# Optimization experiments

Hardware: AMD Instinct MI355X
Metric: run time of the kernel (lower is better)

Reference implementation:

```python
import jax, jax.numpy as jnp
import numpy as np

NH = 16   # num heads
CS = 16   # inner chunk size

def _gelu(x):
    return jax.nn.gelu(x, approximate=True)

def _diff_gelu(x):
    t = jnp.tanh(0.79788456 * x * (1.0 + 0.044715 * x * x))
    return 0.5 * x * ((1.0 - t * t) * (0.79788456 + 0.1070322243 * x * x)) + 0.5 * (1.0 + t)

def _ln_fused_l2_bwd(x, tgt, gamma, beta, eps=1e-6):
    # x, tgt: [B*nh, CS, f]; gamma/beta: [1, nh, 1, f]
    Bnh, N, HF = x.shape
    mu = x.mean(-1, keepdims=True)
    var = x.var(-1, keepdims=True)
    std = jnp.sqrt(var + eps)
    x_hat = (x - mu) / std
    y = gamma * x_hat.reshape(-1, NH, N, HF) + beta
    go = y - tgt.reshape(-1, NH, N, HF)
    gxh = (go * gamma).reshape(Bnh, N, HF)
    return (HF * gxh - gxh.sum(-1, keepdims=True) - x_hat * (gxh * x_hat).sum(-1, keepdims=True)) / (HF * std)

def setup_inputs() -> dict:
    key = jax.random.key(0)
    ks = jax.random.split(key, 8)
    B, nh, f, hf4, n_chunks = 4, NH, 64, 256, 128
    Bnh = B * nh
    XQ = jax.random.normal(ks[0], (n_chunks, Bnh, CS, f), jnp.float32)
    XK = jax.random.normal(ks[1], (n_chunks, Bnh, CS, f), jnp.float32)
    XV = jax.random.normal(ks[2], (n_chunks, Bnh, CS, f), jnp.float32)
    # inner-loop lr coeffs (ilr * token_idx ~ lr/head_dim): small positive
    coeff = jax.random.uniform(ks[3], (n_chunks, Bnh, CS, 1), jnp.float32) * 0.01
    coeff_last = jax.random.uniform(ks[4], (n_chunks, Bnh, 1, 1), jnp.float32) * 0.01
    W1 = jax.random.normal(ks[5], (Bnh, f, hf4), jnp.float32) * 0.02
    b1 = jnp.zeros((Bnh, 1, hf4), jnp.float32)
    W2 = jax.random.normal(ks[6], (Bnh, hf4, f), jnp.float32) * 0.02
    b2 = jnp.zeros((Bnh, 1, f), jnp.float32)
    ln_weight = jnp.ones((1, nh, 1, f), jnp.float32)
    ln_bias = jnp.zeros((1, nh, 1, f), jnp.float32)
    return dict(XQ=XQ, XK=XK, XV=XV, coeff=coeff, coeff_last=coeff_last,
                W1=W1, b1=b1, W2=W2, b2=b2, ln_weight=ln_weight, ln_bias=ln_bias)

def reference(XQ, XK, XV, coeff, coeff_last, W1, b1, W2, b2, ln_weight, ln_bias):
    n_chunks, Bnh, _, f = XQ.shape
    attn_b = jnp.tril(jnp.ones((CS, CS), XQ.dtype))

    def step(carry, inp):
        W1c, b1c, W2c, b2c = carry
        xv, xk, xq, c, cl = inp
        Z1 = xk @ W1c + b1c                      # [Bnh, CS, 4f]
        X2 = _gelu(Z1)
        Z2 = X2 @ W2c + b2c                      # [Bnh, CS, f]
        dZ2 = _ln_fused_l2_bwd(Z2, xv - xk, ln_weight, ln_bias)
        dZ1 = (dZ2 @ W2c.transpose(0, 2, 1)) * _diff_gelu(Z1)
        b1_bar = b1c - c * (attn_b @ dZ1)
        A1 = jnp.tril(xq @ xk.transpose(0, 2, 1))
        Z1_bar = xq @ W1c - c * (A1 @ dZ1) + b1_bar
        X2_bar = _gelu(Z1_bar)
        b2_bar = b2c - c * (attn_b @ dZ2)
        A2 = jnp.tril(X2_bar @ X2.transpose(0, 2, 1))
        Z2_bar = X2_bar @ W2c - c * (A2 @ dZ2) + b2_bar
        W1n = W1c - cl * (xk.transpose(0, 2, 1) @ dZ1)
        W2n = W2c - cl * (X2.transpose(0, 2, 1) @ dZ2)
        return (W1n, b1_bar[:, -1:], W2n, b2_bar[:, -1:]), Z2_bar

    _, Z2_all = jax.lax.scan(step, (W1, b1, W2, b2), (XV, XK, XQ, coeff, coeff_last))
    # [n_chunks, Bnh, CS, f] -> [Bnh, N, f]
    return Z2_all.transpose(1, 0, 2, 3).reshape(Bnh, n_chunks * CS, f)
```

## Files before the change

kernel.cpp:

```cpp
#include <hip/hip_runtime.h>

typedef __attribute__((ext_vector_type(8))) short bf16x8;
typedef __attribute__((ext_vector_type(4))) float f32x4;
typedef __attribute__((ext_vector_type(2))) unsigned int u32x2;

#define MFMA16(a,b,c) __builtin_amdgcn_mfma_f32_16x16x32_bf16(a,b,c,0,0,0)
#define A_GELU 0.7978845608028654f

#define OFF_W1B   0u
#define OFF_W2F   36864u
#define OFF_W2T   70656u
#define OFF_XK    107520u
#define OFF_XQ    109824u
#define OFF_XKT   112128u
#define OFF_X2    115200u
#define OFF_X2B   123648u
#define OFF_DZ2B  132096u
#define OFF_DZ1CT 134400u
#define OFF_DZ2CT 146688u
#define OFF_M1    149760u
#define OFF_M2    150528u
#define OFF_Z2F   151296u
#define OFF_Z2G   155520u
#define OFF_TGT   159744u
#define OFF_B2    162048u
#define OFF_COEF  162560u
#define OFF_CL    162624u
#define SMEM_BYTES 162640u

__device__ __forceinline__ float fast_tanh(float u){
    float e = __expf(2.0f*u);
    return 1.0f - 2.0f/(e + 1.0f);
}
__device__ __forceinline__ float gelu_f(float x){
    float t = fast_tanh(A_GELU*(x + 0.044715f*x*x*x));
    return 0.5f*x*(1.0f+t);
}
__device__ __forceinline__ float dgelu_f(float x){
    float x2 = x*x;
    float t = fast_tanh(A_GELU*x*(1.0f + 0.044715f*x2));
    return 0.5f*x*((1.0f-t*t)*(A_GELU + 0.1070322243f*x2)) + 0.5f*(1.0f+t);
}
__device__ __forceinline__ short f2bf(float f){
    unsigned u = __builtin_bit_cast(unsigned, f);
    u += 0x7FFFu + ((u >> 16) & 1u);
    return (short)(u >> 16);
}
__device__ __forceinline__ float bf2f(unsigned short s){
    unsigned u = ((unsigned)s) << 16;
    return __builtin_bit_cast(float, u);
}
__device__ __forceinline__ unsigned pkbf(float a, float b){
    unsigned r;
    asm("v_cvt_pk_bf16_f32 %0, %1, %2" : "=v"(r) : "v"(a), "v"(b));
    return r;
}
__device__ __forceinline__ bf16x8 ldfrag(const unsigned short* p){
    return *(const bf16x8*)p;
}
__device__ __forceinline__ bf16x8 ldmask16(const unsigned short* row, int hi){
    bf16x8 r = {0,0,0,0,0,0,0,0};
    if (hi < 2) r = *(const bf16x8*)(row + hi*8);
    return r;
}

__global__ __launch_bounds__(512, 1)
void ttt_m2(const float* __restrict__ XQ, const float* __restrict__ XK,
            const float* __restrict__ XV, const float* __restrict__ coeff,
            const float* __restrict__ coeff_last,
            const float* __restrict__ W1g, const float* __restrict__ b1g,
            const float* __restrict__ W2g, const float* __restrict__ b2g,
            const float* __restrict__ gammag, const float* __restrict__ betag,
            float* __restrict__ out)
{
    const int h  = blockIdx.x;
    const int t  = threadIdx.x;
    const int l  = t & 63;
    const int w  = t >> 6;
    const int lo = l & 15;
    const int hi = l >> 4;

    extern __shared__ char smem[];
    unsigned short* sW1bu  = (unsigned short*)(smem + OFF_W1B);
    unsigned short* sW2fu  = (unsigned short*)(smem + OFF_W2F);
    unsigned short* sW2T   = (unsigned short*)(smem + OFF_W2T);
    unsigned short* sxku   = (unsigned short*)(smem + OFF_XK);
    unsigned short* sxqu   = (unsigned short*)(smem + OFF_XQ);
    unsigned short* sxkT   = (unsigned short*)(smem + OFF_XKT);
    unsigned short* sX2u   = (unsigned short*)(smem + OFF_X2);
    unsigned short* sX2bu  = (unsigned short*)(smem + OFF_X2B);
    unsigned short* sdZ2bu = (unsigned short*)(smem + OFF_DZ2B);
    unsigned short* sdZ1ct = (unsigned short*)(smem + OFF_DZ1CT);
    unsigned short* sdZ2ct = (unsigned short*)(smem + OFF_DZ2CT);
    unsigned short* sM1u   = (unsigned short*)(smem + OFF_M1);
    unsigned short* sM2u   = (unsigned short*)(smem + OFF_M2);
    float* sZ2f  = (float*)(smem + OFF_Z2F);
    float* sZ2g  = (float*)(smem + OFF_Z2G);
    unsigned short* stgtu = (unsigned short*)(smem + OFF_TGT);
    float* b2f   = (float*)(smem + OFF_B2);
    float* scoef = (float*)(smem + OFF_COEF);
    float* sCL   = (float*)(smem + OFF_CL);

    const int base1 = h*16384;
    const int base2 = h*16384;

    float mW1[4][2][4];
    float mW2[2][4][4];
    #pragma unroll
    for (int mt = 0; mt < 4; ++mt)
      #pragma unroll
      for (int tix = 0; tix < 2; ++tix)
        #pragma unroll
        for (int reg = 0; reg < 4; ++reg) {
            const int m = mt*16 + hi*4 + reg, n = (2*w + tix)*16 + lo;
            mW1[mt][tix][reg] = W1g[base1 + m*256 + n];
        }
    #pragma unroll
    for (int mi = 0; mi < 2; ++mi)
      #pragma unroll
      for (int nt = 0; nt < 4; ++nt)
        #pragma unroll
        for (int reg = 0; reg < 4; ++reg) {
            const int m = (2*w + mi)*16 + hi*4 + reg, n = nt*16 + lo;
            mW2[mi][nt][reg] = W2g[base2 + m*64 + n];
        }
    float b1reg[2];
    b1reg[0] = b1g[h*256 + (2*w)*16 + lo];
    b1reg[1] = b1g[h*256 + (2*w+1)*16 + lo];

    for (int i = 0; i < 32; ++i) {
        const int idx = i*512 + t;
        const int m = idx >> 8, n = idx & 255;
        sW1bu[n*72 + m] = f2bf(W1g[base1 + idx]);
    }
    for (int i = 0; i < 32; ++i) {
        const int idx = i*512 + t;
        const int hf = idx >> 6, f = idx & 63;
        const short v = f2bf(W2g[base2 + idx]);
        sW2fu[f*264 + hf] = v;
        sW2T[hf*72 + f]   = v;
    }
    if (t < 64) b2f[t] = b2g[h*64 + t];

    const float gj = gammag[(h & 15)*64 + l];
    const float bj = betag [(h & 15)*64 + l];

    {
        const int r0 = w*2;
        const float xk0 = XK[h*1024 + r0*64 + l],     xq0 = XQ[h*1024 + r0*64 + l];
        const float xk1 = XK[h*1024 + (r0+1)*64 + l], xq1 = XQ[h*1024 + (r0+1)*64 + l];
        const float xv0 = XV[h*1024 + r0*64 + l],     xv1 = XV[h*1024 + (r0+1)*64 + l];
        const unsigned pkk = pkbf(xk0, xk1), pkq = pkbf(xq0, xq1);
        const unsigned pkt = pkbf(xv0 - xk0, xv1 - xk1);
        sxku[r0*72 + l]     = (unsigned short)pkk;
        sxku[(r0+1)*72 + l] = (unsigned short)(pkk >> 16);
        sxqu[r0*72 + l]     = (unsigned short)pkq;
        sxqu[(r0+1)*72 + l] = (unsigned short)(pkq >> 16);
        *(unsigned*)&sxkT[l*24 + r0] = pkk;
        stgtu[r0*72 + l]     = (unsigned short)pkt;
        stgtu[(r0+1)*72 + l] = (unsigned short)(pkt >> 16);
        if (t < 16)  scoef[t] = coeff[h*16 + t];
        if (t == 16) sCL[0]   = coeff_last[h];
    }
    __syncthreads();

    for (int ci = 0; ci < 128; ++ci) {
        const float clv = sCL[0];
        const float c15 = scoef[15];
        float crs[4];
        #pragma unroll
        for (int reg = 0; reg < 4; ++reg) crs[reg] = scoef[hi*4 + reg];

        float pxk[4], pxq[4], pxv[4];
        float pcf = 0.f, pcl = 0.f;
        if (w >= 4 && ci < 127) {
            const int cb1 = (ci + 1)*65536 + h*1024;
            const int r0 = (w - 4)*4;
            #pragma unroll
            for (int i = 0; i < 4; ++i) {
                pxk[i] = XK[cb1 + (r0 + i)*64 + l];
                pxq[i] = XQ[cb1 + (r0 + i)*64 + l];
                pxv[i] = XV[cb1 + (r0 + i)*64 + l];
            }
            const int u = t - 256;
            if (u < 16)  pcf = coeff[(ci + 1)*1024 + h*16 + u];
            if (u == 16) pcl = coeff_last[(ci + 1)*64 + h];
        }

        float z1s[8];
        bf16x8 afk0 = ldfrag(sxku + lo*72 + hi*8);
        bf16x8 afk1 = ldfrag(sxku + lo*72 + 32 + hi*8);
        #pragma unroll
        for (int tix = 0; tix < 2; ++tix) {
            const int n = (2*w + tix)*16 + lo;
            f32x4 acc = {b1reg[tix], b1reg[tix], b1reg[tix], b1reg[tix]};
            acc = MFMA16(afk0, ldfrag(sW1bu + n*72 + hi*8), acc);
            acc = MFMA16(afk1, ldfrag(sW1bu + n*72 + 32 + hi*8), acc);
            float g[4];
            #pragma unroll
            for (int reg = 0; reg < 4; ++reg) {
                z1s[tix*4 + reg] = acc[reg];
                g[reg] = gelu_f(acc[reg]);
            }
            const unsigned p01 = pkbf(g[0], g[1]), p23 = pkbf(g[2], g[3]);
            sX2u[(hi*4+0)*264 + n] = (unsigned short)p01;
            sX2u[(hi*4+1)*264 + n] = (unsigned short)(p01 >> 16);
            sX2u[(hi*4+2)*264 + n] = (unsigned short)p23;
            sX2u[(hi*4+3)*264 + n] = (unsigned short)(p23 >> 16);
        }
        if (w == 0) {
            bf16x8 aq0 = ldfrag(sxqu + lo*72 + hi*8);
            bf16x8 aq1 = ldfrag(sxqu + lo*72 + 32 + hi*8);
            f32x4 a1 = {0.f, 0.f, 0.f, 0.f};
            a1 = MFMA16(aq0, afk0, a1);
            a1 = MFMA16(aq1, afk1, a1);
            #pragma unroll
            for (int reg = 0; reg < 4; ++reg) {
                const int r = hi*4 + reg;
                const float v = (lo <= r) ? (-crs[reg]*(a1[reg] + 1.0f)) : 0.0f;
                sM1u[r*24 + lo] = f2bf(v);
            }
        }
        #pragma unroll
        for (int mi = 0; mi < 2; ++mi)
          #pragma unroll
          for (int nt = 0; nt < 4; ++nt) {
                const int n = nt*16 + lo, m0 = (2*w + mi)*16 + hi*4;
                const unsigned p01 = pkbf(mW2[mi][nt][0], mW2[mi][nt][1]);
                const unsigned p23 = pkbf(mW2[mi][nt][2], mW2[mi][nt][3]);
                *(u32x2*)&sW2fu[n*264 + m0] = (u32x2){p01, p23};
                sW2T[(m0+0)*72 + n] = (unsigned short)p01;
                sW2T[(m0+1)*72 + n] = (unsigned short)(p01 >> 16);
                sW2T[(m0+2)*72 + n] = (unsigned short)p23;
                sW2T[(m0+3)*72 + n] = (unsigned short)(p23 >> 16);
          }
        __syncthreads();

        const int tile = w & 3, kh = w >> 2;
        const int nf = tile*16 + lo;
        {
            f32x4 acc;
            if (kh == 0) {
                const float b2v = b2f[(ci & 1)*64 + nf];
                acc = (f32x4){b2v, b2v, b2v, b2v};
            } else acc = (f32x4){0.f, 0.f, 0.f, 0.f};
            #pragma unroll
            for (int s = 0; s < 4; ++s) {
                const int k = (kh*4 + s)*32 + hi*8;
                acc = MFMA16(ldfrag(sX2u + lo*264 + k),
                             ldfrag(sW2fu + nf*264 + k), acc);
            }
            float* dst = (kh == 0) ? sZ2g : sZ2f;
            #pragma unroll
            for (int reg = 0; reg < 4; ++reg)
                dst[(hi*4 + reg)*66 + nf] = acc[reg];
        }
        __syncthreads();

        {
            float dzp[2];
            #pragma unroll
            for (int i = 0; i < 2; ++i) {
                const int r = w*2 + i;
                const float z2 = sZ2f[r*66 + l] + sZ2g[r*66 + l];
                float s1 = z2, s2 = z2*z2;
                #pragma unroll
                for (int m = 1; m < 64; m <<= 1) { s1 += __shfl_xor(s1, m); s2 += __shfl_xor(s2, m); }
                const float mu   = s1*(1.0f/64.0f);
                const float var  = s2*(1.0f/64.0f) - mu*mu;
                const float rstd = rsqrtf(var + 1e-6f);
                const float xh   = (z2 - mu)*rstd;
                const float go   = gj*xh + bj - bf2f(stgtu[r*72 + l]);
                const float gg   = go*gj;
                float u1 = gg, u2 = gg*xh;
                #pragma unroll
                for (int m = 1; m < 64; m <<= 1) { u1 += __shfl_xor(u1, m); u2 += __shfl_xor(u2, m); }
                dzp[i] = (64.0f*gg - u1 - xh*u2)*(rstd*(1.0f/64.0f));
            }
            const unsigned pk = pkbf(dzp[0], dzp[1]);
            sdZ2bu[(w*2)*72 + l]   = (unsigned short)pk;
            sdZ2bu[(w*2+1)*72 + l] = (unsigned short)(pk >> 16);
            *(unsigned*)&sdZ2ct[l*24 + w*2] = pk;
        }
        __syncthreads();

        float b1old[2];
        {
            bf16x8 ad0 = ldfrag(sdZ2bu + lo*72 + hi*8);
            bf16x8 ad1 = ldfrag(sdZ2bu + lo*72 + 32 + hi*8);
            #pragma unroll
            for (int tix = 0; tix < 2; ++tix) {
                const int n = (2*w + tix)*16 + lo;
                f32x4 acc = {0.f, 0.f, 0.f, 0.f};
                acc = MFMA16(ad0, ldfrag(sW2T + n*72 + hi*8), acc);
                acc = MFMA16(ad1, ldfrag(sW2T + n*72 + 32 + hi*8), acc);
                float dv[4], cs = 0.f;
                #pragma unroll
                for (int reg = 0; reg < 4; ++reg) {
                    dv[reg] = acc[reg]*dgelu_f(z1s[tix*4 + reg]);
                    cs += dv[reg];
                }
                *(u32x2*)&sdZ1ct[n*24 + hi*4] =
                    (u32x2){pkbf(dv[0], dv[1]), pkbf(dv[2], dv[3])};
                cs += __shfl_xor(cs, 16);
                cs += __shfl_xor(cs, 32);
                b1old[tix] = b1reg[tix];
                b1reg[tix] -= c15*cs;
            }
        }
        __syncthreads();

        {
            bf16x8 aq0 = ldfrag(sxqu + lo*72 + hi*8);
            bf16x8 aq1 = ldfrag(sxqu + lo*72 + 32 + hi*8);
            bf16x8 am1 = ldmask16(sM1u + lo*24, hi);
            #pragma unroll
            for (int tix = 0; tix < 2; ++tix) {
                const int n = (2*w + tix)*16 + lo;
                f32x4 acc = {b1old[tix], b1old[tix], b1old[tix], b1old[tix]};
                acc = MFMA16(aq0, ldfrag(sW1bu + n*72 + hi*8), acc);
                acc = MFMA16(aq1, ldfrag(sW1bu + n*72 + 32 + hi*8), acc);
                acc = MFMA16(am1, ldmask16(sdZ1ct + n*24, hi), acc);
                float g[4];
                #pragma unroll
                for (int reg = 0; reg < 4; ++reg) g[reg] = gelu_f(acc[reg]);
                const unsigned p01 = pkbf(g[0], g[1]), p23 = pkbf(g[2], g[3]);
                sX2bu[(hi*4+0)*264 + n] = (unsigned short)p01;
                sX2bu[(hi*4+1)*264 + n] = (unsigned short)(p01 >> 16);
                sX2bu[(hi*4+2)*264 + n] = (unsigned short)p23;
                sX2bu[(hi*4+3)*264 + n] = (unsigned short)(p23 >> 16);
            }
            bf16x8 bz0 = ldmask16(sdZ1ct + ((2*w)*16 + lo)*24, hi);
            bf16x8 bz1 = ldmask16(sdZ1ct + ((2*w+1)*16 + lo)*24, hi);
            #pragma unroll
            for (int mt = 0; mt < 4; ++mt) {
                bf16x8 axt = ldmask16(sxkT + (mt*16 + lo)*24, hi);
                f32x4 z4 = {0.f,0.f,0.f,0.f};
                f32x4 u0 = MFMA16(axt, bz0, z4);
                f32x4 u1 = MFMA16(axt, bz1, z4);
                #pragma unroll
                for (int reg = 0; reg < 4; ++reg) {
                    mW1[mt][0][reg] -= clv*u0[reg];
                    mW1[mt][1][reg] -= clv*u1[reg];
                }
            }
        }
        __syncthreads();

        {
            bf16x8 bz2[4];
            #pragma unroll
            for (int nt = 0; nt < 4; ++nt)
                bz2[nt] = ldmask16(sdZ2ct + (nt*16 + lo)*24, hi);
            #pragma unroll
            for (int mi = 0; mi < 2; ++mi) {
                const int mt = 2*w + mi;
                bf16x8 ax2 = (bf16x8){0,0,0,0,0,0,0,0};
                if (l < 32) {
                    #pragma unroll
                    for (int j = 0; j < 8; ++j)
                        ax2[j] = (short)sX2u[(hi*8 + j)*264 + (mt*16 + lo)];
                }
                #pragma unroll
                for (int nt = 0; nt < 4; ++nt) {
                    f32x4 z4 = {0.f,0.f,0.f,0.f};
                    f32x4 u = MFMA16(ax2, bz2[nt], z4);
                    #pragma unroll
                    for (int reg = 0; reg < 4; ++reg)
                        mW2[mi][nt][reg] -= clv*u[reg];
                }
            }
            if (w == 0) {
                f32x4 a2 = {0.f,0.f,0.f,0.f};
                #pragma unroll
                for (int ks = 0; ks < 8; ++ks) {
                    const int k = ks*32 + hi*8;
                    a2 = MFMA16(ldfrag(sX2bu + lo*264 + k),
                                ldfrag(sX2u + lo*264 + k), a2);
                }
                #pragma unroll
                for (int reg = 0; reg < 4; ++reg) {
                    const int r = hi*4 + reg;
                    const float v = (lo <= r) ? (-crs[reg]*(a2[reg] + 1.0f)) : 0.0f;
                    sM2u[r*24 + lo] = f2bf(v);
                }
            }
            if (w == 1) {
                float cs = 0.f;
                #pragma unroll
                for (int k = 0; k < 16; ++k) cs += bf2f(sdZ2bu[k*72 + l]);
                b2f[((ci + 1) & 1)*64 + l] = b2f[(ci & 1)*64 + l] - c15*cs;
            }
            #pragma unroll
            for (int mt = 0; mt < 4; ++mt)
              #pragma unroll
              for (int tix = 0; tix < 2; ++tix) {
                    const int n = (2*w + tix)*16 + lo, m0 = mt*16 + hi*4;
                    *(u32x2*)&sW1bu[n*72 + m0] =
                        (u32x2){pkbf(mW1[mt][tix][0], mW1[mt][tix][1]),
                                pkbf(mW1[mt][tix][2], mW1[mt][tix][3])};
              }
        }
        __syncthreads();

        if (w < 4) {
            const int nf2 = w*16 + lo;
            const float b2v = b2f[(ci & 1)*64 + nf2];
            f32x4 acc = {b2v, b2v, b2v, b2v};
            #pragma unroll
            for (int s = 0; s < 8; ++s) {
                const int k0 = s*32 + hi*8;
                acc = MFMA16(ldfrag(sX2bu + lo*264 + k0),
                             ldfrag(sW2fu + nf2*264 + k0), acc);
            }
            acc = MFMA16(ldmask16(sM2u + lo*24, hi),
                         ldmask16(sdZ2ct + nf2*24, hi), acc);
            #pragma unroll
            for (int reg = 0; reg < 4; ++reg)
                out[h*131072 + (ci*16 + hi*4 + reg)*64 + nf2] = acc[reg];
        } else if (ci < 127) {
            const int r0 = (w - 4)*4;
            #pragma unroll
            for (int p = 0; p < 2; ++p) {
                const int r = r0 + 2*p;
                const unsigned pkk = pkbf(pxk[2*p], pxk[2*p+1]);
                const unsigned pkq = pkbf(pxq[2*p], pxq[2*p+1]);
                const unsigned pkt = pkbf(pxv[2*p] - pxk[2*p], pxv[2*p+1] - pxk[2*p+1]);
                sxku[r*72 + l]     = (unsigned short)pkk;
                sxku[(r+1)*72 + l] = (unsigned short)(pkk >> 16);
                sxqu[r*72 + l]     = (unsigned short)pkq;
                sxqu[(r+1)*72 + l] = (unsigned short)(pkq >> 16);
                *(unsigned*)&sxkT[l*24 + r] = pkk;
                stgtu[r*72 + l]     = (unsigned short)pkt;
                stgtu[(r+1)*72 + l] = (unsigned short)(pkt >> 16);
            }
            const int u = t - 256;
            if (u < 16)  scoef[u] = pcf;
            if (u == 16) sCL[0]   = pcl;
        }
        __syncthreads();
    }
}

extern "C" void kernel_launch(void* const* d_in, const int* in_sizes, int n_in,
                              void* d_out, int out_size, void* d_ws, size_t ws_size,
                              hipStream_t stream) {
    const float* XQ  = (const float*)d_in[0];
    const float* XK  = (const float*)d_in[1];
    const float* XV  = (const float*)d_in[2];
    const float* cf  = (const float*)d_in[3];
    const float* cfl = (const float*)d_in[4];
    const float* W1  = (const float*)d_in[5];
    const float* b1  = (const float*)d_in[6];
    const float* W2  = (const float*)d_in[7];
    const float* b2  = (const float*)d_in[8];
    const float* gam = (const float*)d_in[9];
    const float* bet = (const float*)d_in[10];
    float* o = (float*)d_out;

    hipFuncSetAttribute((const void*)ttt_m2,
                        hipFuncAttributeMaxDynamicSharedMemorySize, SMEM_BYTES);
    ttt_m2<<<64, 512, SMEM_BYTES, stream>>>(XQ, XK, XV, cf, cfl, W1, b1, W2, b2, gam, bet, o);
}
```

Measured before the change: 866.9 us.

## Keep a transposed W2 copy in registers and build X2 fragments via shuffles

Adds a second register-resident copy of W2 in transposed fragment layout, updated by its own MFMAs each chunk. The transposed shared-memory copy of W2 can then be written with packed 8-byte stores instead of four scalar 2-byte stores. The X2 operand for the W2 update is now built from the GELU values kept in registers, using cross-lane shuffles rather than strided scalar LDS reads. In exchange it uses 32 more registers per thread and eight more MFMAs per chunk, which could lower occupancy or cause spills.

After: 1.497 ms. +72.7%, slower.

```diff
diff --git a/kernel.cpp b/kernel.cpp
--- a/kernel.cpp
+++ b/kernel.cpp
@@ -3,6 +3,7 @@
 typedef __attribute__((ext_vector_type(8))) short bf16x8;
 typedef __attribute__((ext_vector_type(4))) float f32x4;
 typedef __attribute__((ext_vector_type(2))) unsigned int u32x2;
+typedef __attribute__((ext_vector_type(4))) unsigned int u32x4;
 
 #define MFMA16(a,b,c) __builtin_amdgcn_mfma_f32_16x16x32_bf16(a,b,c,0,0,0)
 #define A_GELU 0.7978845608028654f
@@ -106,6 +107,7 @@
 
     float mW1[4][2][4];
     float mW2[2][4][4];
+    float mW2T[4][2][4];
     #pragma unroll
     for (int mt = 0; mt < 4; ++mt)
       #pragma unroll
@@ -123,6 +125,15 @@
         for (int reg = 0; reg < 4; ++reg) {
             const int m = (2*w + mi)*16 + hi*4 + reg, n = nt*16 + lo;
             mW2[mi][nt][reg] = W2g[base2 + m*64 + n];
+        }
+    #pragma unroll
+    for (int ft = 0; ft < 4; ++ft)
+      #pragma unroll
+      for (int tix = 0; tix < 2; ++tix)
+        #pragma unroll
+        for (int reg = 0; reg < 4; ++reg) {
+            const int f = ft*16 + hi*4 + reg, hf = (2*w + tix)*16 + lo;
+            mW2T[ft][tix][reg] = W2g[base2 + hf*64 + f];
         }
     float b1reg[2];
     b1reg[0] = b1g[h*256 + (2*w)*16 + lo];
@@ -188,6 +199,7 @@
         }
 
         float z1s[8];
+        unsigned px2[2][2];
         bf16x8 afk0 = ldfrag(sxku + lo*72 + hi*8);
         bf16x8 afk1 = ldfrag(sxku + lo*72 + 32 + hi*8);
         #pragma unroll
@@ -203,6 +215,7 @@
                 g[reg] = gelu_f(acc[reg]);
             }
             const unsigned p01 = pkbf(g[0], g[1]), p23 = pkbf(g[2], g[3]);
+            px2[tix][0] = p01; px2[tix][1] = p23;
             sX2u[(hi*4+0)*264 + n] = (unsigned short)p01;
             sX2u[(hi*4+1)*264 + n] = (unsigned short)(p01 >> 16);
             sX2u[(hi*4+2)*264 + n] = (unsigned short)p23;
@@ -226,13 +239,18 @@
           #pragma unroll
           for (int nt = 0; nt < 4; ++nt) {
                 const int n = nt*16 + lo, m0 = (2*w + mi)*16 + hi*4;
-                const unsigned p01 = pkbf(mW2[mi][nt][0], mW2[mi][nt][1]);
-                const unsigned p23 = pkbf(mW2[mi][nt][2], mW2[mi][nt][3]);
-                *(u32x2*)&sW2fu[n*264 + m0] = (u32x2){p01, p23};
-                sW2T[(m0+0)*72 + n] = (unsigned short)p01;
-                sW2T[(m0+1)*72 + n] = (unsigned short)(p01 >> 16);
-                sW2T[(m0+2)*72 + n] = (unsigned short)p23;
-                sW2T[(m0+3)*72 + n] = (unsigned short)(p23 >> 16);
+                *(u32x2*)&sW2fu[n*264 + m0] =
+                    (u32x2){pkbf(mW2[mi][nt][0], mW2[mi][nt][1]),
+                            pkbf(mW2[mi][nt][2], mW2[mi][nt][3])};
+          }
+        #pragma unroll
+        for (int ft = 0; ft < 4; ++ft)
+          #pragma unroll
+          for (int tix = 0; tix < 2; ++tix) {
+                const int hf = (2*w + tix)*16 + lo, f0 = ft*16 + hi*4;
+                *(u32x2*)&sW2T[hf*72 + f0] =
+                    (u32x2){pkbf(mW2T[ft][tix][0], mW2T[ft][tix][1]),
+                            pkbf(mW2T[ft][tix][2], mW2T[ft][tix][3])};
           }
         __syncthreads();
 
@@ -352,24 +370,39 @@
             #pragma unroll
             for (int nt = 0; nt < 4; ++nt)
                 bz2[nt] = ldmask16(sdZ2ct + (nt*16 + lo)*24, hi);
-            #pragma unroll
-            for (int mi = 0; mi < 2; ++mi) {
-                const int mt = 2*w + mi;
-                bf16x8 ax2 = (bf16x8){0,0,0,0,0,0,0,0};
-                if (l < 32) {
-                    #pragma unroll
-                    for (int j = 0; j < 8; ++j)
-                        ax2[j] = (short)sX2u[(hi*8 + j)*264 + (mt*16 + lo)];
-                }
+            bf16x8 xf[2];
+            {
+                const int base = lo + 32*(hi & 1);
+                #pragma unroll
+                for (int tix = 0; tix < 2; ++tix) {
+                    unsigned w0 = (unsigned)__shfl((int)px2[tix][0], base);
+                    unsigned w1 = (unsigned)__shfl((int)px2[tix][1], base);
+                    unsigned w2 = (unsigned)__shfl((int)px2[tix][0], base + 16);
+                    unsigned w3 = (unsigned)__shfl((int)px2[tix][1], base + 16);
+                    if (hi >= 2) { w0 = 0; w1 = 0; w2 = 0; w3 = 0; }
+                    xf[tix] = __builtin_bit_cast(bf16x8, (u32x4){w0, w1, w2, w3});
+                }
+            }
+            #pragma unroll
+            for (int mi = 0; mi < 2; ++mi)
                 #pragma unroll
                 for (int nt = 0; nt < 4; ++nt) {
                     f32x4 z4 = {0.f,0.f,0.f,0.f};
-                    f32x4 u = MFMA16(ax2, bz2[nt], z4);
+                    f32x4 u = MFMA16(xf[mi], bz2[nt], z4);
                     #pragma unroll
                     for (int reg = 0; reg < 4; ++reg)
                         mW2[mi][nt][reg] -= clv*u[reg];
                 }
-            }
+            #pragma unroll
+            for (int ft = 0; ft < 4; ++ft)
+                #pragma unroll
+                for (int tix = 0; tix < 2; ++tix) {
+                    f32x4 z4 = {0.f,0.f,0.f,0.f};
+                    f32x4 u = MFMA16(bz2[ft], xf[tix], z4);
+                    #pragma unroll
+                    for (int reg = 0; reg < 4; ++reg)
+                        mW2T[ft][tix][reg] -= clv*u[reg];
+                }
             if (w == 0) {
                 f32x4 a2 = {0.f,0.f,0.f,0.f};
                 #pragma unroll
```
